# Kernel tuning notes

Hardware: AMD Instinct MI355X
Metric: run time of the kernel (lower is better)

## Reference

```python
import jax, jax.numpy as jnp
import numpy as np

TEMPERATURE = 1.0
CLAMP = 10.0

def setup_inputs() -> dict:
    key = jax.random.key(0)
    k1, k2, kw, kb, km = jax.random.split(key, 5)
    B, N1, N2, D = 8, 2048, 2048, 256
    features1 = jax.random.normal(k1, (B, N1, D), dtype=jnp.float32)
    features2 = jax.random.normal(k2, (B, N2, D), dtype=jnp.float32)
    # Linear(D, D) params (torch convention: y = x @ W.T + b)
    W = jax.random.normal(kw, (D, D), dtype=jnp.float32) * (1.0 / np.sqrt(D))
    b = jax.random.normal(kb, (D,), dtype=jnp.float32) * 0.02
    # learnable metric matrix (initialized near identity, small perturbation)
    metric = jnp.eye(D, dtype=jnp.float32) + 0.01 * jax.random.normal(km, (D, D), dtype=jnp.float32)
    return {"features1": features1, "features2": features2, "W": W, "b": b, "metric": metric}

def reference(features1, features2, W, b, metric):
    # Linear transform (torch nn.Linear: x @ W.T + b)
    f1 = features1 @ W.T + b  # (B, N1, D)
    f2 = features2 @ W.T + b  # (B, N2, D)
    M = (metric + metric.T) * 0.5  # symmetrized metric (D, D)
    # Mahalanobis distance^2 expanded: d(x,y) = xMx + yMy - 2 xMy (valid since M symmetric)
    f1M = f1 @ M                                      # (B, N1, D)
    f2M = f2 @ M                                      # (B, N2, D)
    q1 = jnp.sum(f1M * f1, axis=-1)                   # (B, N1)
    q2 = jnp.sum(f2M * f2, axis=-1)                   # (B, N2)
    cross = jnp.einsum('bnd,bmd->bnm', f1M, f2)       # (B, N1, N2)
    dist_sq = q1[:, :, None] + q2[:, None, :] - 2.0 * cross
    stable = jnp.clip(-dist_sq / TEMPERATURE, -CLAMP, CLAMP)
    return jnp.exp(stable)
```

## Files before the change

kernel.cpp:

```cpp
#include <hip/hip_runtime.h>

#define DD 256
#define NROW 2048
#define TROWS 16384

typedef __attribute__((ext_vector_type(8))) short short8;
typedef __attribute__((ext_vector_type(4))) float f32x4;

__device__ __forceinline__ unsigned short f2bf(float f) {
  unsigned int u = __float_as_uint(f);
  u += 0x7FFFu + ((u >> 16) & 1u);
  return (unsigned short)(u >> 16);
}

__device__ __forceinline__ void gload_lds16(const unsigned short* g, unsigned short* l) {
  __builtin_amdgcn_global_load_lds(
      (const __attribute__((address_space(1))) unsigned int*)(const void*)g,
      (__attribute__((address_space(3))) unsigned int*)(void*)l,
      16, 0, 0);
}


__global__ void k_prep(const float* __restrict__ metric, const float* __restrict__ W,
                       const float* __restrict__ bvec,
                       unsigned short* __restrict__ Wbf, unsigned short* __restrict__ WpT,
                       float* __restrict__ bp)
{
  __shared__ float msrow[DD];
  __shared__ float red[DD];
  const int e = blockIdx.x, d = threadIdx.x;
  msrow[d] = 0.5f * (metric[e*DD + d] + metric[d*DD + e]);
  Wbf[e*DD + d] = f2bf(W[e*DD + d]);
  __syncthreads();
  float acc = 0.f;
  for (int j = 0; j < DD; ++j) acc += msrow[j] * W[j*DD + d];
  WpT[e*DD + d] = f2bf(acc);
  red[d] = msrow[d] * bvec[d];
  __syncthreads();
  for (int s = 128; s; s >>= 1) { if (d < s) red[d] += red[d + s]; __syncthreads(); }
  if (d == 0) bp[e] = red[0];
}

__global__ __launch_bounds__(256, 2)
void k_fgemm(const float* __restrict__ x1, const float* __restrict__ x2,
             const unsigned short* __restrict__ B1, const unsigned short* __restrict__ B2,
             const float* __restrict__ bb, const float* __restrict__ bpv,
             unsigned short* __restrict__ o1, unsigned short* __restrict__ o2,
             float* __restrict__ qp1, float* __restrict__ qp2)
{
  __shared__ __align__(16) unsigned short As[2][64*32];
  __shared__ __align__(16) unsigned short B1s[2][256*32];
  __shared__ __align__(16) unsigned short B2s[2][256*32];

  const int tid  = threadIdx.x;
  const int lane = tid & 63;
  const int wave = tid >> 6;
  const int row0 = blockIdx.x * 64;
  const int z    = blockIdx.y;

  const float* X       = z ? x2 : x1;
  unsigned short* outp = z ? o2 : o1;
  float* qp            = z ? qp2 : qp1;

  f32x4 accF[4][4], accM[4][4];
#pragma unroll
  for (int m = 0; m < 4; ++m)
#pragma unroll
    for (int n = 0; n < 4; ++n) { accF[m][n] = (f32x4){0,0,0,0}; accM[m][n] = (f32x4){0,0,0,0}; }

  const int ar   = tid >> 2;
  const int ako  = (tid & 3) * 8;
  const int akos = (((tid & 3) ^ ((ar >> 1) & 3))) * 8;
  const int lrow  = lane >> 2;
  const int lkswz = (((lane & 3) ^ ((lrow >> 1) & 3))) * 8;

#define STAGE_B(buf, k0) do { \
  _Pragma("unroll") \
  for (int c = 0; c < 4; ++c) { \
    const int chunk = wave * 4 + c; \
    const int rb = (chunk*16 + lrow)*DD + (k0) + lkswz; \
    gload_lds16(B1 + rb, &B1s[buf][chunk*512]); \
    gload_lds16(B2 + rb, &B2s[buf][chunk*512]); \
  } } while (0)

#define LOAD_A(k0) \
  float4 a0 = *(const float4*)(X + (long long)(row0 + ar)*DD + (k0) + ako); \
  float4 a1 = *(const float4*)(X + (long long)(row0 + ar)*DD + (k0) + ako + 4)

#define CVT_WRITE_A(buf) do { \
  union { unsigned short us[8]; int4 v; } uu; \
  uu.us[0]=f2bf(a0.x); uu.us[1]=f2bf(a0.y); uu.us[2]=f2bf(a0.z); uu.us[3]=f2bf(a0.w); \
  uu.us[4]=f2bf(a1.x); uu.us[5]=f2bf(a1.y); uu.us[6]=f2bf(a1.z); uu.us[7]=f2bf(a1.w); \
  *(int4*)&As[buf][ar*32 + akos] = uu.v; } while (0)

  { LOAD_A(0); STAGE_B(0, 0); CVT_WRITE_A(0); }
  __syncthreads();

  const int lr  = lane & 15;
  const int lks = (((lane >> 4) ^ ((lr >> 1) & 3))) * 8;

#pragma unroll
  for (int kt = 0; kt < 8; ++kt) {
    const int cur = kt & 1;
    if (kt < 7) {
      const int k0 = (kt + 1) * 32;
      LOAD_A(k0);
      STAGE_B(cur ^ 1, k0);
      short8 af[4];
#pragma unroll
      for (int m = 0; m < 4; ++m) af[m] = *(const short8*)&As[cur][(m*16 + lr)*32 + lks];
#pragma unroll
      for (int n = 0; n < 4; ++n) {
        const short8 b1 = *(const short8*)&B1s[cur][(wave*64 + n*16 + lr)*32 + lks];
        const short8 b2 = *(const short8*)&B2s[cur][(wave*64 + n*16 + lr)*32 + lks];
#pragma unroll
        for (int m = 0; m < 4; ++m) {
          accF[m][n] = __builtin_amdgcn_mfma_f32_16x16x32_bf16(af[m], b1, accF[m][n], 0, 0, 0);
          accM[m][n] = __builtin_amdgcn_mfma_f32_16x16x32_bf16(af[m], b2, accM[m][n], 0, 0, 0);
        }
      }
      CVT_WRITE_A(cur ^ 1);
    } else {
      short8 af[4];
#pragma unroll
      for (int m = 0; m < 4; ++m) af[m] = *(const short8*)&As[cur][(m*16 + lr)*32 + lks];
#pragma unroll
      for (int n = 0; n < 4; ++n) {
        const short8 b1 = *(const short8*)&B1s[cur][(wave*64 + n*16 + lr)*32 + lks];
        const short8 b2 = *(const short8*)&B2s[cur][(wave*64 + n*16 + lr)*32 + lks];
#pragma unroll
        for (int m = 0; m < 4; ++m) {
          accF[m][n] = __builtin_amdgcn_mfma_f32_16x16x32_bf16(af[m], b1, accF[m][n], 0, 0, 0);
          accM[m][n] = __builtin_amdgcn_mfma_f32_16x16x32_bf16(af[m], b2, accM[m][n], 0, 0, 0);
        }
      }
    }
    __syncthreads();
  }

  float bbv[4], bpv4[4];
#pragma unroll
  for (int n = 0; n < 4; ++n) {
    const int coll = wave*64 + n*16 + (lane & 15);
    bbv[n]  = bb[coll];
    bpv4[n] = bpv[coll];
  }
#pragma unroll
  for (int m = 0; m < 4; ++m) {
#pragma unroll
    for (int r = 0; r < 4; ++r) {
      const int rowl = m*16 + (lane >> 4)*4 + r;
      float p = 0.f;
#pragma unroll
      for (int n = 0; n < 4; ++n) {
        const int coll = wave*64 + n*16 + (lane & 15);
        const float fv  = accF[m][n][r] + bbv[n];
        const float fMv = accM[m][n][r] + bpv4[n];
        p += fv * fMv;
        outp[(long long)(row0 + rowl)*DD + coll] = f2bf(z ? fv : fMv);
      }
      p += __shfl_xor(p, 1); p += __shfl_xor(p, 2);
      p += __shfl_xor(p, 4); p += __shfl_xor(p, 8);
      if ((lane & 15) == 0) qp[wave*TROWS + row0 + rowl] = p;
    }
  }
#undef STAGE_B
#undef LOAD_A
#undef CVT_WRITE_A
}

__global__ __launch_bounds__(256, 2)
void k_cross(const unsigned short* __restrict__ f1M, const unsigned short* __restrict__ f2,
             const float* __restrict__ qp1, const float* __restrict__ qp2,
             float* __restrict__ out)
{
  __shared__ __align__(16) unsigned short As[2][128*32];
  __shared__ __align__(16) unsigned short Bs[2][128*32];
  __shared__ float q1s[128];
  __shared__ float q2s[128];

  const int tid  = threadIdx.x;
  const int lane = tid & 63;
  const int wave = tid >> 6;
  const int wr = wave >> 1;
  const int wc = wave & 1;

  const int bid = blockIdx.x;
  const int z  = bid & 7;
  const int t  = bid >> 3;
  const int bx = t & 15;
  const int by = t >> 4;
  const int row0 = by * 128;
  const int col0 = bx * 128;

  const unsigned short* A = f1M + (long long)z * NROW * DD;
  const unsigned short* B = f2  + (long long)z * NROW * DD;

  if (tid < 128) {
    const int rg = z*NROW + row0 + tid;
    q1s[tid] = qp1[rg] + qp1[TROWS + rg] + qp1[2*TROWS + rg] + qp1[3*TROWS + rg];
  } else {
    const int cg = z*NROW + col0 + (tid - 128);
    q2s[tid-128] = qp2[cg] + qp2[TROWS + cg] + qp2[2*TROWS + cg] + qp2[3*TROWS + cg];
  }

  f32x4 acc[4][4];
#pragma unroll
  for (int m = 0; m < 4; ++m)
#pragma unroll
    for (int n = 0; n < 4; ++n) acc[m][n] = (f32x4){0,0,0,0};

  const int lrow  = lane >> 2;
  const int lkswz = (((lane & 3) ^ ((lrow >> 1) & 3))) * 8;

#define STAGE_C(buf, k0) do { \
  _Pragma("unroll") \
  for (int c = 0; c < 2; ++c) { \
    const int chunk = wave * 2 + c; \
    gload_lds16(A + (long long)(row0 + chunk*16 + lrow)*DD + (k0) + lkswz, &As[buf][chunk*512]); \
    gload_lds16(B + (long long)(col0 + chunk*16 + lrow)*DD + (k0) + lkswz, &Bs[buf][chunk*512]); \
  } } while (0)

  STAGE_C(0, 0);
  __syncthreads();

  const int lr  = lane & 15;
  const int lks = (((lane >> 4) ^ ((lr >> 1) & 3))) * 8;

#pragma unroll
  for (int kt = 0; kt < 8; ++kt) {
    const int cur = kt & 1;
    if (kt < 7) STAGE_C(cur ^ 1, (kt + 1) * 32);
    short8 af[4];
#pragma unroll
    for (int m = 0; m < 4; ++m) af[m] = *(const short8*)&As[cur][(wr*64 + m*16 + lr)*32 + lks];
#pragma unroll
    for (int n = 0; n < 4; ++n) {
      const short8 bfr = *(const short8*)&Bs[cur][(wc*64 + n*16 + lr)*32 + lks];
#pragma unroll
      for (int m = 0; m < 4; ++m)
        acc[m][n] = __builtin_amdgcn_mfma_f32_16x16x32_bf16(af[m], bfr, acc[m][n], 0, 0, 0);
    }
    __syncthreads();
  }

  float* outz = out + (long long)z * NROW * NROW;
#pragma unroll
  for (int m = 0; m < 4; ++m) {
#pragma unroll
    for (int r = 0; r < 4; ++r) {
      const int rowl = wr*64 + m*16 + (lane >> 4)*4 + r;
#pragma unroll
      for (int n = 0; n < 4; ++n) {
        const int coll = wc*64 + n*16 + (lane & 15);
        const float dsq = q1s[rowl] + q2s[coll] - 2.0f * acc[m][n][r];
        const float sc = fminf(fmaxf(-dsq, -10.0f), 10.0f);
        outz[(long long)(row0 + rowl)*NROW + (col0 + coll)] = __expf(sc);
      }
    }
  }
#undef STAGE_C
}

extern "C" void kernel_launch(void* const* d_in, const int* in_sizes, int n_in,
                              void* d_out, int out_size, void* d_ws, size_t ws_size,
                              hipStream_t stream) {
  const float* x1     = (const float*)d_in[0];
  const float* x2     = (const float*)d_in[1];
  const float* W      = (const float*)d_in[2];
  const float* bv     = (const float*)d_in[3];
  const float* metric = (const float*)d_in[4];
  float* out = (float*)d_out;

  if (ws_size < 20000000) return;
  unsigned short* p   = (unsigned short*)d_ws;
  unsigned short* f1M = p; p += (size_t)TROWS*DD;
  unsigned short* f2  = p; p += (size_t)TROWS*DD;
  unsigned short* Wbf = p; p += DD*DD;
  unsigned short* WpT = p; p += DD*DD;
  float* fp  = (float*)p;
  float* qp1 = fp; fp += 4*TROWS;
  float* qp2 = fp; fp += 4*TROWS;
  float* bp  = fp; fp += 256;

  k_prep<<<256, 256, 0, stream>>>(metric, W, bv, Wbf, WpT, bp);
  dim3 gf(256, 2);
  k_fgemm<<<gf, 256, 0, stream>>>(x1, x2, Wbf, WpT, bv, bp, f1M, f2, qp1, qp2);
  k_cross<<<2048, 256, 0, stream>>>(f1M, f2, qp1, qp2, out);
}
```

Before: 70.31 us.

## Enlarge cross-GEMM tile to 256x256 with 8 waves and split-K pipelined staging

Replaces the 128x128, 4-wave cross-distance kernel with a 256x256, 8-wave kernel that stages K in two 32-wide halves per 64-wide step. It uses explicit vmcnt waits, raw barriers and setprio around MFMA groups to overlap global-to-LDS loads with compute. Larger tiles halve operand reloads from global memory. The cost is about 128KB of LDS per block and only 512 blocks, which lowers occupancy, and the epilogue stays dominated by the large fp32 output writes.

```diff
diff --git a/kernel.cpp b/kernel.cpp
--- a/kernel.cpp
+++ b/kernel.cpp
@@ -6,6 +6,7 @@
 
 typedef __attribute__((ext_vector_type(8))) short short8;
 typedef __attribute__((ext_vector_type(4))) float f32x4;
+typedef __attribute__((ext_vector_type(4))) int i32x4;
 
 __device__ __forceinline__ unsigned short f2bf(float f) {
   unsigned int u = __float_as_uint(f);
@@ -19,7 +20,6 @@
       (__attribute__((address_space(3))) unsigned int*)(void*)l,
       16, 0, 0);
 }
-
 
 __global__ void k_prep(const float* __restrict__ metric, const float* __restrict__ W,
                        const float* __restrict__ bvec,
@@ -84,14 +84,14 @@
   } } while (0)
 
 #define LOAD_A(k0) \
-  float4 a0 = *(const float4*)(X + (long long)(row0 + ar)*DD + (k0) + ako); \
-  float4 a1 = *(const float4*)(X + (long long)(row0 + ar)*DD + (k0) + ako + 4)
+  f32x4 a0 = *(const f32x4*)(X + (long long)(row0 + ar)*DD + (k0) + ako); \
+  f32x4 a1 = *(const f32x4*)(X + (long long)(row0 + ar)*DD + (k0) + ako + 4)
 
 #define CVT_WRITE_A(buf) do { \
-  union { unsigned short us[8]; int4 v; } uu; \
+  union { unsigned short us[8]; i32x4 v; } uu; \
   uu.us[0]=f2bf(a0.x); uu.us[1]=f2bf(a0.y); uu.us[2]=f2bf(a0.z); uu.us[3]=f2bf(a0.w); \
   uu.us[4]=f2bf(a1.x); uu.us[5]=f2bf(a1.y); uu.us[6]=f2bf(a1.z); uu.us[7]=f2bf(a1.w); \
-  *(int4*)&As[buf][ar*32 + akos] = uu.v; } while (0)
+  *(i32x4*)&As[buf][ar*32 + akos] = uu.v; } while (0)
 
   { LOAD_A(0); STAGE_B(0, 0); CVT_WRITE_A(0); }
   __syncthreads();
@@ -169,97 +169,129 @@
 #undef CVT_WRITE_A
 }
 
-__global__ __launch_bounds__(256, 2)
-void k_cross(const unsigned short* __restrict__ f1M, const unsigned short* __restrict__ f2,
-             const float* __restrict__ qp1, const float* __restrict__ qp2,
-             float* __restrict__ out)
+__global__ __launch_bounds__(512, 2)
+void k_cross8(const unsigned short* __restrict__ f1M, const unsigned short* __restrict__ f2,
+              const float* __restrict__ qp1, const float* __restrict__ qp2,
+              float* __restrict__ out)
 {
-  __shared__ __align__(16) unsigned short As[2][128*32];
-  __shared__ __align__(16) unsigned short Bs[2][128*32];
-  __shared__ float q1s[128];
-  __shared__ float q2s[128];
+  __shared__ __align__(16) unsigned short Ak[2][2][256*32];
+  __shared__ __align__(16) unsigned short Bk[2][2][256*32];
+  __shared__ float q1s[256], q2s[256];
 
   const int tid  = threadIdx.x;
   const int lane = tid & 63;
   const int wave = tid >> 6;
-  const int wr = wave >> 1;
-  const int wc = wave & 1;
+  const int wr = wave >> 2;
+  const int wc = wave & 3;
 
   const int bid = blockIdx.x;
   const int z  = bid & 7;
-  const int t  = bid >> 3;
-  const int bx = t & 15;
-  const int by = t >> 4;
-  const int row0 = by * 128;
-  const int col0 = bx * 128;
-
-  const unsigned short* A = f1M + (long long)z * NROW * DD;
-  const unsigned short* B = f2  + (long long)z * NROW * DD;
-
-  if (tid < 128) {
+  const int t2 = bid >> 3;
+  const int col0 = (t2 & 7) * 256;
+  const int row0 = (t2 >> 3) * 256;
+
+  const unsigned short* Abase = f1M + (long long)z * NROW * DD + (long long)row0 * DD;
+  const unsigned short* Bbase = f2  + (long long)z * NROW * DD + (long long)col0 * DD;
+
+  if (tid < 256) {
     const int rg = z*NROW + row0 + tid;
     q1s[tid] = qp1[rg] + qp1[TROWS + rg] + qp1[2*TROWS + rg] + qp1[3*TROWS + rg];
   } else {
-    const int cg = z*NROW + col0 + (tid - 128);
-    q2s[tid-128] = qp2[cg] + qp2[TROWS + cg] + qp2[2*TROWS + cg] + qp2[3*TROWS + cg];
-  }
-
-  f32x4 acc[4][4];
-#pragma unroll
-  for (int m = 0; m < 4; ++m)
+    const int cg = z*NROW + col0 + (tid - 256);
+    q2s[tid-256] = qp2[cg] + qp2[TROWS + cg] + qp2[2*TROWS + cg] + qp2[3*TROWS + cg];
+  }
+
+  const int srow = lane >> 2;
+  const int sk8  = ((lane & 3) ^ ((srow >> 1) & 3)) * 8;
+  const int lr16 = lane & 15;
+  const int lko  = (((lane >> 4) ^ ((lane >> 1) & 3))) * 8;
+
+#define STAGE_K(MatPtr, ldsArr, kkv, dbuf, kt) do { \
+  _Pragma("unroll") \
+  for (int c = 0; c < 2; ++c) { \
+    const int rbase = c*128 + wave*16; \
+    gload_lds16(MatPtr + (long long)(rbase + srow)*DD + (kt)*64 + (kkv)*32 + sk8, \
+                &ldsArr[kkv][dbuf][rbase*32]); \
+  } } while (0)
+
+#define LDA4(mq, kkv, d) do { \
+  _Pragma("unroll") \
+  for (int i = 0; i < 4; ++i) \
+    a_[i] = *(const short8*)&Ak[kkv][d][(wr*128 + ((mq)*4+i)*16 + lr16)*32 + lko]; \
+  } while (0)
+
+#define LDB4(kkv, d) do { \
+  _Pragma("unroll") \
+  for (int i = 0; i < 4; ++i) \
+    b_[i] = *(const short8*)&Bk[kkv][d][(wc*64 + i*16 + lr16)*32 + lko]; \
+  } while (0)
+
+#define MFMA16(mq) do { \
+  __builtin_amdgcn_s_setprio(1); \
+  _Pragma("unroll") \
+  for (int n = 0; n < 4; ++n) \
+    _Pragma("unroll") \
+    for (int i = 0; i < 4; ++i) \
+      acc[(mq)*4+i][n] = __builtin_amdgcn_mfma_f32_16x16x32_bf16(a_[i], b_[n], acc[(mq)*4+i][n], 0, 0, 0); \
+  __builtin_amdgcn_s_setprio(0); \
+  } while (0)
+
+  f32x4 acc[8][4];
+#pragma unroll
+  for (int m = 0; m < 8; ++m)
 #pragma unroll
     for (int n = 0; n < 4; ++n) acc[m][n] = (f32x4){0,0,0,0};
 
-  const int lrow  = lane >> 2;
-  const int lkswz = (((lane & 3) ^ ((lrow >> 1) & 3))) * 8;
-
-#define STAGE_C(buf, k0) do { \
-  _Pragma("unroll") \
-  for (int c = 0; c < 2; ++c) { \
-    const int chunk = wave * 2 + c; \
-    gload_lds16(A + (long long)(row0 + chunk*16 + lrow)*DD + (k0) + lkswz, &As[buf][chunk*512]); \
-    gload_lds16(B + (long long)(col0 + chunk*16 + lrow)*DD + (k0) + lkswz, &Bs[buf][chunk*512]); \
-  } } while (0)
-
-  STAGE_C(0, 0);
-  __syncthreads();
-
-  const int lr  = lane & 15;
-  const int lks = (((lane >> 4) ^ ((lr >> 1) & 3))) * 8;
-
-#pragma unroll
-  for (int kt = 0; kt < 8; ++kt) {
-    const int cur = kt & 1;
-    if (kt < 7) STAGE_C(cur ^ 1, (kt + 1) * 32);
-    short8 af[4];
-#pragma unroll
-    for (int m = 0; m < 4; ++m) af[m] = *(const short8*)&As[cur][(wr*64 + m*16 + lr)*32 + lks];
-#pragma unroll
-    for (int n = 0; n < 4; ++n) {
-      const short8 bfr = *(const short8*)&Bs[cur][(wc*64 + n*16 + lr)*32 + lks];
-#pragma unroll
-      for (int m = 0; m < 4; ++m)
-        acc[m][n] = __builtin_amdgcn_mfma_f32_16x16x32_bf16(af[m], bfr, acc[m][n], 0, 0, 0);
-    }
-    __syncthreads();
+  STAGE_K(Abase, Ak, 0, 0, 0);
+  STAGE_K(Bbase, Bk, 0, 0, 0);
+  STAGE_K(Abase, Ak, 1, 0, 0);
+  STAGE_K(Bbase, Bk, 1, 0, 0);
+
+  short8 a_[4], b_[4];
+
+#pragma unroll
+  for (int kt = 0; kt < 4; ++kt) {
+    const int d = kt & 1;
+    asm volatile("s_waitcnt vmcnt(4)" ::: "memory");
+    __builtin_amdgcn_s_barrier();
+    __builtin_amdgcn_sched_barrier(0);
+    if (kt < 3) STAGE_K(Abase, Ak, 0, d ^ 1, kt + 1);
+    LDA4(0, 0, d); LDB4(0, d);
+    MFMA16(0);
+    if (kt < 3) STAGE_K(Bbase, Bk, 0, d ^ 1, kt + 1);
+    LDA4(1, 0, d);
+    MFMA16(1);
+    if (kt < 3) { asm volatile("s_waitcnt vmcnt(4)" ::: "memory"); }
+    else        { asm volatile("s_waitcnt vmcnt(0)" ::: "memory"); }
+    __builtin_amdgcn_s_barrier();
+    __builtin_amdgcn_sched_barrier(0);
+    if (kt < 3) STAGE_K(Abase, Ak, 1, d ^ 1, kt + 1);
+    LDA4(1, 1, d); LDB4(1, d);
+    MFMA16(1);
+    if (kt < 3) STAGE_K(Bbase, Bk, 1, d ^ 1, kt + 1);
+    LDA4(0, 1, d);
+    MFMA16(0);
   }
 
   float* outz = out + (long long)z * NROW * NROW;
 #pragma unroll
-  for (int m = 0; m < 4; ++m) {
+  for (int m = 0; m < 8; ++m) {
 #pragma unroll
     for (int r = 0; r < 4; ++r) {
-      const int rowl = wr*64 + m*16 + (lane >> 4)*4 + r;
+      const int rowl = wr*128 + m*16 + (lane >> 4)*4 + r;
 #pragma unroll
       for (int n = 0; n < 4; ++n) {
-        const int coll = wc*64 + n*16 + (lane & 15);
-        const float dsq = q1s[rowl] + q2s[coll] - 2.0f * acc[m][n][r];
+        const int cloc = wc*64 + n*16 + (lane & 15);
+        const float dsq = q1s[rowl] + q2s[cloc] - 2.0f * acc[m][n][r];
         const float sc = fminf(fmaxf(-dsq, -10.0f), 10.0f);
-        outz[(long long)(row0 + rowl)*NROW + (col0 + coll)] = __expf(sc);
+        outz[(long long)(row0 + rowl)*NROW + (col0 + cloc)] = __expf(sc);
       }
     }
   }
-#undef STAGE_C
+#undef STAGE_K
+#undef LDA4
+#undef LDB4
+#undef MFMA16
 }
 
 extern "C" void kernel_launch(void* const* d_in, const int* in_sizes, int n_in,
@@ -286,5 +318,5 @@
   k_prep<<<256, 256, 0, stream>>>(metric, W, bv, Wbf, WpT, bp);
   dim3 gf(256, 2);
   k_fgemm<<<gf, 256, 0, stream>>>(x1, x2, Wbf, WpT, bv, bp, f1M, f2, qp1, qp2);
-  k_cross<<<2048, 256, 0, stream>>>(f1M, f2, qp1, qp2, out);
-}
+  k_cross8<<<512, 512, 0, stream>>>(f1M, f2, qp1, qp2, out);
+}
```

New measurement: 72.14 us. 2.6% more time.

## Fold bias-invariant metric into single Gram matrix, halving feature GEMM work

Applied to the files above, without the earlier changes.

Because the bias cancels in the distance (f1-f2), the kernel precomputes G = W^T * sym(M) * W and computes y1 = x1·G and q = x·G·x directly from raw inputs. The cross GEMM then uses y1 against a bf16 copy of x2. This removes one of the two MFMA accumulator sets and one B staging buffer in the feature GEMM, allowing higher occupancy. The trade-off is a heavier prep kernel with strided metric reads, plus extra global reads of fp32 x rows in the epilogue.

```diff
diff --git a/kernel.cpp b/kernel.cpp
--- a/kernel.cpp
+++ b/kernel.cpp
@@ -6,6 +6,7 @@
 
 typedef __attribute__((ext_vector_type(8))) short short8;
 typedef __attribute__((ext_vector_type(4))) float f32x4;
+typedef __attribute__((ext_vector_type(4))) int i32x4;
 
 __device__ __forceinline__ unsigned short f2bf(float f) {
   unsigned int u = __float_as_uint(f);
@@ -20,37 +21,32 @@
       16, 0, 0);
 }
 
-
-__global__ void k_prep(const float* __restrict__ metric, const float* __restrict__ W,
-                       const float* __restrict__ bvec,
-                       unsigned short* __restrict__ Wbf, unsigned short* __restrict__ WpT,
-                       float* __restrict__ bp)
+__global__ void k_prepG(const float* __restrict__ M, const float* __restrict__ W,
+                        unsigned short* __restrict__ Gbf)
 {
-  __shared__ float msrow[DD];
-  __shared__ float red[DD];
+  __shared__ float wcol[DD];
+  __shared__ float srow[DD];
   const int e = blockIdx.x, d = threadIdx.x;
-  msrow[d] = 0.5f * (metric[e*DD + d] + metric[d*DD + e]);
-  Wbf[e*DD + d] = f2bf(W[e*DD + d]);
-  __syncthreads();
-  float acc = 0.f;
-  for (int j = 0; j < DD; ++j) acc += msrow[j] * W[j*DD + d];
-  WpT[e*DD + d] = f2bf(acc);
-  red[d] = msrow[d] * bvec[d];
-  __syncthreads();
-  for (int s = 128; s; s >>= 1) { if (d < s) red[d] += red[d + s]; __syncthreads(); }
-  if (d == 0) bp[e] = red[0];
-}
-
-__global__ __launch_bounds__(256, 2)
-void k_fgemm(const float* __restrict__ x1, const float* __restrict__ x2,
-             const unsigned short* __restrict__ B1, const unsigned short* __restrict__ B2,
-             const float* __restrict__ bb, const float* __restrict__ bpv,
-             unsigned short* __restrict__ o1, unsigned short* __restrict__ o2,
+  wcol[d] = W[d*DD + e];
+  __syncthreads();
+  float a = 0.f, b = 0.f;
+  for (int k = 0; k < DD; ++k) a += wcol[k] * M[k*DD + d];
+  for (int k = 0; k < DD; ++k) b += M[d*DD + k] * wcol[k];
+  srow[d] = 0.5f * (a + b);
+  __syncthreads();
+  float g = 0.f;
+  for (int j = 0; j < DD; ++j) g += srow[j] * W[j*DD + d];
+  Gbf[e*DD + d] = f2bf(g);
+}
+
+__global__ __launch_bounds__(256, 3)
+void k_ygemm(const float* __restrict__ x1, const float* __restrict__ x2,
+             const unsigned short* __restrict__ Gb,
+             unsigned short* __restrict__ y1, unsigned short* __restrict__ x2b,
              float* __restrict__ qp1, float* __restrict__ qp2)
 {
   __shared__ __align__(16) unsigned short As[2][64*32];
-  __shared__ __align__(16) unsigned short B1s[2][256*32];
-  __shared__ __align__(16) unsigned short B2s[2][256*32];
+  __shared__ __align__(16) unsigned short Bs[2][256*32];
 
   const int tid  = threadIdx.x;
   const int lane = tid & 63;
@@ -58,15 +54,14 @@
   const int row0 = blockIdx.x * 64;
   const int z    = blockIdx.y;
 
-  const float* X       = z ? x2 : x1;
-  unsigned short* outp = z ? o2 : o1;
-  float* qp            = z ? qp2 : qp1;
-
-  f32x4 accF[4][4], accM[4][4];
+  const float* X = z ? x2 : x1;
+  float* qp      = z ? qp2 : qp1;
+
+  f32x4 acc[4][4];
 #pragma unroll
   for (int m = 0; m < 4; ++m)
 #pragma unroll
-    for (int n = 0; n < 4; ++n) { accF[m][n] = (f32x4){0,0,0,0}; accM[m][n] = (f32x4){0,0,0,0}; }
+    for (int n = 0; n < 4; ++n) acc[m][n] = (f32x4){0,0,0,0};
 
   const int ar   = tid >> 2;
   const int ako  = (tid & 3) * 8;
@@ -78,22 +73,22 @@
   _Pragma("unroll") \
   for (int c = 0; c < 4; ++c) { \
     const int chunk = wave * 4 + c; \
-    const int rb = (chunk*16 + lrow)*DD + (k0) + lkswz; \
-    gload_lds16(B1 + rb, &B1s[buf][chunk*512]); \
-    gload_lds16(B2 + rb, &B2s[buf][chunk*512]); \
+    gload_lds16(Gb + (chunk*16 + lrow)*DD + (k0) + lkswz, &Bs[buf][chunk*512]); \
   } } while (0)
 
 #define LOAD_A(k0) \
-  float4 a0 = *(const float4*)(X + (long long)(row0 + ar)*DD + (k0) + ako); \
-  float4 a1 = *(const float4*)(X + (long long)(row0 + ar)*DD + (k0) + ako + 4)
-
-#define CVT_WRITE_A(buf) do { \
-  union { unsigned short us[8]; int4 v; } uu; \
+  f32x4 a0 = *(const f32x4*)(X + (long long)(row0 + ar)*DD + (k0) + ako); \
+  f32x4 a1 = *(const f32x4*)(X + (long long)(row0 + ar)*DD + (k0) + ako + 4)
+
+#define CVT_WRITE_A(buf, k0) do { \
+  union { unsigned short us[8]; i32x4 v; } uu; \
   uu.us[0]=f2bf(a0.x); uu.us[1]=f2bf(a0.y); uu.us[2]=f2bf(a0.z); uu.us[3]=f2bf(a0.w); \
   uu.us[4]=f2bf(a1.x); uu.us[5]=f2bf(a1.y); uu.us[6]=f2bf(a1.z); uu.us[7]=f2bf(a1.w); \
-  *(int4*)&As[buf][ar*32 + akos] = uu.v; } while (0)
-
-  { LOAD_A(0); STAGE_B(0, 0); CVT_WRITE_A(0); }
+  *(i32x4*)&As[buf][ar*32 + akos] = uu.v; \
+  if (z) *(i32x4*)&x2b[(long long)(row0 + ar)*DD + (k0) + ako] = uu.v; \
+  } while (0)
+
+  { LOAD_A(0); STAGE_B(0, 0); CVT_WRITE_A(0, 0); }
   __syncthreads();
 
   const int lr  = lane & 15;
@@ -111,53 +106,40 @@
       for (int m = 0; m < 4; ++m) af[m] = *(const short8*)&As[cur][(m*16 + lr)*32 + lks];
 #pragma unroll
       for (int n = 0; n < 4; ++n) {
-        const short8 b1 = *(const short8*)&B1s[cur][(wave*64 + n*16 + lr)*32 + lks];
-        const short8 b2 = *(const short8*)&B2s[cur][(wave*64 + n*16 + lr)*32 + lks];
-#pragma unroll
-        for (int m = 0; m < 4; ++m) {
-          accF[m][n] = __builtin_amdgcn_mfma_f32_16x16x32_bf16(af[m], b1, accF[m][n], 0, 0, 0);
-          accM[m][n] = __builtin_amdgcn_mfma_f32_16x16x32_bf16(af[m], b2, accM[m][n], 0, 0, 0);
-        }
-      }
-      CVT_WRITE_A(cur ^ 1);
+        const short8 b1 = *(const short8*)&Bs[cur][(wave*64 + n*16 + lr)*32 + lks];
+#pragma unroll
+        for (int m = 0; m < 4; ++m)
+          acc[m][n] = __builtin_amdgcn_mfma_f32_16x16x32_bf16(af[m], b1, acc[m][n], 0, 0, 0);
+      }
+      CVT_WRITE_A(cur ^ 1, k0);
     } else {
       short8 af[4];
 #pragma unroll
       for (int m = 0; m < 4; ++m) af[m] = *(const short8*)&As[cur][(m*16 + lr)*32 + lks];
 #pragma unroll
       for (int n = 0; n < 4; ++n) {
-        const short8 b1 = *(const short8*)&B1s[cur][(wave*64 + n*16 + lr)*32 + lks];
-        const short8 b2 = *(const short8*)&B2s[cur][(wave*64 + n*16 + lr)*32 + lks];
-#pragma unroll
-        for (int m = 0; m < 4; ++m) {
-          accF[m][n] = __builtin_amdgcn_mfma_f32_16x16x32_bf16(af[m], b1, accF[m][n], 0, 0, 0);
-          accM[m][n] = __builtin_amdgcn_mfma_f32_16x16x32_bf16(af[m], b2, accM[m][n], 0, 0, 0);
-        }
+        const short8 b1 = *(const short8*)&Bs[cur][(wave*64 + n*16 + lr)*32 + lks];
+#pragma unroll
+        for (int m = 0; m < 4; ++m)
+          acc[m][n] = __builtin_amdgcn_mfma_f32_16x16x32_bf16(af[m], b1, acc[m][n], 0, 0, 0);
       }
     }
     __syncthreads();
   }
 
-  float bbv[4], bpv4[4];
-#pragma unroll
-  for (int n = 0; n < 4; ++n) {
-    const int coll = wave*64 + n*16 + (lane & 15);
-    bbv[n]  = bb[coll];
-    bpv4[n] = bpv[coll];
-  }
 #pragma unroll
   for (int m = 0; m < 4; ++m) {
 #pragma unroll
     for (int r = 0; r < 4; ++r) {
       const int rowl = m*16 + (lane >> 4)*4 + r;
+      const float* xrow = X + (long long)(row0 + rowl)*DD;
       float p = 0.f;
 #pragma unroll
       for (int n = 0; n < 4; ++n) {
         const int coll = wave*64 + n*16 + (lane & 15);
-        const float fv  = accF[m][n][r] + bbv[n];
-        const float fMv = accM[m][n][r] + bpv4[n];
-        p += fv * fMv;
-        outp[(long long)(row0 + rowl)*DD + coll] = f2bf(z ? fv : fMv);
+        const float yv = acc[m][n][r];
+        p += yv * xrow[coll];
+        if (!z) y1[(long long)(row0 + rowl)*DD + coll] = f2bf(yv);
       }
       p += __shfl_xor(p, 1); p += __shfl_xor(p, 2);
       p += __shfl_xor(p, 4); p += __shfl_xor(p, 8);
@@ -170,7 +152,7 @@
 }
 
 __global__ __launch_bounds__(256, 2)
-void k_cross(const unsigned short* __restrict__ f1M, const unsigned short* __restrict__ f2,
+void k_cross(const unsigned short* __restrict__ y1, const unsigned short* __restrict__ x2b,
              const float* __restrict__ qp1, const float* __restrict__ qp2,
              float* __restrict__ out)
 {
@@ -193,8 +175,8 @@
   const int row0 = by * 128;
   const int col0 = bx * 128;
 
-  const unsigned short* A = f1M + (long long)z * NROW * DD;
-  const unsigned short* B = f2  + (long long)z * NROW * DD;
+  const unsigned short* A = y1  + (long long)z * NROW * DD;
+  const unsigned short* B = x2b + (long long)z * NROW * DD;
 
   if (tid < 128) {
     const int rg = z*NROW + row0 + tid;
@@ -268,23 +250,20 @@
   const float* x1     = (const float*)d_in[0];
   const float* x2     = (const float*)d_in[1];
   const float* W      = (const float*)d_in[2];
-  const float* bv     = (const float*)d_in[3];
   const float* metric = (const float*)d_in[4];
   float* out = (float*)d_out;
 
-  if (ws_size < 20000000) return;
+  if (ws_size < 18000000) return;
   unsigned short* p   = (unsigned short*)d_ws;
-  unsigned short* f1M = p; p += (size_t)TROWS*DD;
-  unsigned short* f2  = p; p += (size_t)TROWS*DD;
-  unsigned short* Wbf = p; p += DD*DD;
-  unsigned short* WpT = p; p += DD*DD;
+  unsigned short* y1  = p; p += (size_t)TROWS*DD;
+  unsigned short* x2b = p; p += (size_t)TROWS*DD;
+  unsigned short* Gbf = p; p += DD*DD;
   float* fp  = (float*)p;
   float* qp1 = fp; fp += 4*TROWS;
   float* qp2 = fp; fp += 4*TROWS;
-  float* bp  = fp; fp += 256;
-
-  k_prep<<<256, 256, 0, stream>>>(metric, W, bv, Wbf, WpT, bp);
+
+  k_prepG<<<256, 256, 0, stream>>>(metric, W, Gbf);
   dim3 gf(256, 2);
-  k_fgemm<<<gf, 256, 0, stream>>>(x1, x2, Wbf, WpT, bv, bp, f1M, f2, qp1, qp2);
-  k_cross<<<2048, 256, 0, stream>>>(f1M, f2, qp1, qp2, out);
-}
+  k_ygemm<<<gf, 256, 0, stream>>>(x1, x2, Gbf, y1, x2b, qp1, qp2);
+  k_cross<<<2048, 256, 0, stream>>>(y1, x2b, qp1, qp2, out);
+}
```

Result: slower. 79.87 us (+13.6%).
